# Optimization experiments

Hardware: AMD Instinct MI355X
Metric: run time of the kernel (lower is better)

Reference implementation:

```python
import jax, jax.numpy as jnp
import numpy as np

NUM_HEADS = 12
LEVEL = 16
SOFTMAX_STEP = 6.0  # spiking_softmax.step

def _if_init(shape):
    # torch lazily inits q = zeros + 0.5, acc_q = zeros
    return (jnp.full(shape, 0.5, jnp.float32), jnp.zeros(shape, jnp.float32))

def _if_step(state, x, pos_max, neg_min):
    # IFNeuron with q_threshold = 1.0, borrow = 0.0 (all t-branches collapse to q += x.detach())
    q, acc = state
    q = q + jax.lax.stop_gradient(x)
    acc = jnp.round(acc)
    pos = (q - 1.0 >= 0.0) & (acc < pos_max)
    neg = (q < 0.0) & (acc > neg_min)
    out = jnp.where(pos, 1.0, jnp.where(neg, -1.0, 0.0)).astype(jnp.float32)
    return (q - out, acc + out), out

def _forward(x, w_qkv, w_proj):
    T, B, N, C = x.shape
    H = NUM_HEADS
    D = C // H
    scale = D ** -0.5
    pos_s, neg_s = LEVEL // 2 - 1, -(LEVEL // 2)  # sym=True IF neurons
    pos_u, neg_u = LEVEL // 2 - 1, 0              # sym=False (attn_softmax_IF)

    carry = (
        _if_init((B, H, N, D)), _if_init((B, H, N, D)), _if_init((B, H, N, D)),  # q/k/v IF
        _if_init((B, H, N, N)), _if_init((B, H, N, N)),                           # attn IF, softmax IF
        _if_init((B, H, N, D)), _if_init((B, N, C)),                              # after-attn IF, proj IF
        jnp.zeros((B, H, N, N), jnp.float32), jnp.zeros((B, H, N, N), jnp.float32),  # Ssoftmax X, Y_pre
    )

    def step(carry, xs):
        xt, t = xs
        qif, kif, vif, aif, sif, oif, pif, sm_X, sm_Y = carry
        qkv = (xt @ w_qkv.T).reshape(B, N, 3, H, D).transpose(2, 0, 3, 1, 4)  # [3,B,H,N,D]
        qif, q = _if_step(qif, qkv[0], pos_s, neg_s)
        kif, k = _if_step(kif, qkv[1], pos_s, neg_s)
        vif, v = _if_step(vif, qkv[2], pos_s, neg_s)
        q_s = q * scale
        q_acc = qif[1] * scale  # acc_q * scale * q_threshold (thr=1)
        k_acc = kif[1]
        # AttentionMulti incremental-sum QK^T: q_sum@k^T + q@k_sum^T - q@k^T
        attn = (jnp.einsum('bhnd,bhmd->bhnm', q_acc, k)
                + jnp.einsum('bhnd,bhmd->bhnm', q_s, k_acc)
                - jnp.einsum('bhnd,bhmd->bhnm', q_s, k))
        aif, attn = _if_step(aif, attn, pos_s, neg_s)
        # spiking_softmax: delta of (scaled) softmax over accumulated logits
        sm_X = sm_X + attn
        Y = jax.nn.softmax(sm_X, axis=-1) * jnp.minimum(t / SOFTMAX_STEP, 1.0)
        attn = Y - sm_Y
        sm_Y = Y
        sif, attn = _if_step(sif, attn, pos_u, neg_u)
        # AttentionMulti1 incremental-sum attn@V: a_sum@v + a@v_sum - a@v
        out = (jnp.einsum('bhnm,bhmd->bhnd', sif[1], v)
               + jnp.einsum('bhnm,bhmd->bhnd', attn, vif[1])
               - jnp.einsum('bhnm,bhmd->bhnd', attn, v))
        oif, out = _if_step(oif, out, pos_s, neg_s)
        out = out.transpose(0, 2, 1, 3).reshape(B, N, C) @ w_proj.T
        pif, out = _if_step(pif, out, pos_s, neg_s)
        return (qif, kif, vif, aif, sif, oif, pif, sm_X, sm_Y), out

    ts = jnp.arange(1, T + 1, dtype=jnp.float32)
    _, ys = jax.lax.scan(step, carry, (x, ts))
    return ys  # [T, B, N, C] spike outputs per timestep

def setup_inputs():
    key = jax.random.key(0)
    k1, k2, k3 = jax.random.split(key, 3)
    T, B, N, C = 8, 8, 512, 768
    x = jax.random.normal(k1, (T, B, N, C), jnp.float32)
    w_qkv = jax.random.normal(k2, (3 * C, C), jnp.float32) / np.sqrt(C)
    w_proj = jax.random.normal(k3, (C, C), jnp.float32) / np.sqrt(C)
    return {"x": x, "w_qkv": w_qkv, "w_proj": w_proj}

def reference(x, w_qkv, w_proj):
    return _forward(x, w_qkv, w_proj)
```

## Files before the change

### kernel.cpp

```cpp
#include <hip/hip_runtime.h>
#include <stdint.h>

typedef __attribute__((ext_vector_type(4))) float f32x4;
typedef __attribute__((ext_vector_type(8))) short s16x8;
typedef __attribute__((ext_vector_type(8))) char  s8x8;
typedef __attribute__((ext_vector_type(16))) char s8x16;
typedef unsigned short u16;

constexpr int    Tn  = 8;
constexpr int    Nn  = 512;
constexpr int    Cn  = 768;
constexpr int    Dn  = 64;
constexpr int    BHn = 96;
constexpr int    BNn = 4096;
constexpr int    C3n = 2304;
constexpr size_t BHND = 3145728;
constexpr size_t BHNN = 25165824;
constexpr size_t BNC  = 3145728;

__device__ int8_t g_A1[(size_t)Tn * BHND * 2];
__device__ int8_t g_B1[(size_t)Tn * BHND * 2];
__device__ short  g_S16[(size_t)Tn * BHNN];
__device__ int8_t g_v8 [(size_t)Tn * BHND];
__device__ int8_t g_vd8[(size_t)Tn * BHND];
__device__ int8_t g_vT[(size_t)Tn * BHn * Dn * 1024];
__device__ int8_t g_sifa8[(size_t)Tn * BHNN];
__device__ int8_t g_spk8[(size_t)Tn * BHNN];
__device__ short  g_pv16[(size_t)Tn * BHND];
__device__ int8_t g_osp8i[(size_t)BNn * Tn * Cn];

static __device__ __forceinline__ u16 f2bf(float f) {
    union { float f; unsigned int u; } v; v.f = f;
    return (u16)(v.u >> 16);
}

static __device__ __forceinline__ s16x8 cvt_i8_bf16x8(const int8_t* p) {
    s8x8 v = *(const s8x8*)p;
    s16x8 r;
#pragma unroll
    for (int j = 0; j < 8; ++j) r[j] = (short)f2bf((float)v[j]);
    return r;
}

static __device__ __forceinline__ void st2i8(int8_t* p, int v0, int v1) {
    *(short*)p = (short)((v0 & 0xff) | (v1 << 8));
}

static __device__ __forceinline__ float if_sym(float x, float& q, int& a) {
    float q2 = q + x;
    bool pos = ((q2 - 1.0f) >= 0.0f) && (a < 7);
    bool neg = (q2 < 0.0f) && (a > -8);
    float out = pos ? 1.0f : (neg ? -1.0f : 0.0f);
    q = q2 - out;
    a += (int)out;
    return out;
}

__global__ __launch_bounds__(256) void gemm_qkv_fused(
    const float* __restrict__ X, const float* __restrict__ B)
{
    __shared__ __align__(16) float As[16][132];
    __shared__ __align__(16) float Bs[16][100];
    const int tid = threadIdx.x;
    const int m0 = blockIdx.y * 128;
    const int j0 = blockIdx.x * 96;
    const int ty = tid >> 4, tx = tid & 15;

    float acc[8][6];
#pragma unroll
    for (int i = 0; i < 8; ++i)
#pragma unroll
        for (int j = 0; j < 6; ++j) acc[i][j] = 0.0f;

    for (int k0 = 0; k0 < Cn; k0 += 16) {
#pragma unroll
        for (int u = 0; u < 2; ++u) {
            int f = tid + u * 256;
            int row = f >> 2;
            int c4 = (f & 3) * 4;
            int m = m0 + row;
            int t = m & 7, bn = m >> 3;
            int b = bn >> 9, n = bn & 511;
            const float* xr = X + ((size_t)((t * 8 + b) * Nn + n)) * Cn;
            float4 av = *(const float4*)(xr + k0 + c4);
            As[c4 + 0][row] = av.x; As[c4 + 1][row] = av.y;
            As[c4 + 2][row] = av.z; As[c4 + 3][row] = av.w;
        }
#pragma unroll
        for (int u = 0; u < 3; ++u) {
            int f = tid + u * 256;
            int row = f >> 3;
            int c2 = (f & 7) * 2;
            float2 bv = *(const float2*)(B + (size_t)(j0 + row) * Cn + k0 + c2);
            Bs[c2][row] = bv.x; Bs[c2 + 1][row] = bv.y;
        }
        __syncthreads();
#pragma unroll
        for (int k = 0; k < 16; ++k) {
            alignas(16) float a[8];
            alignas(8)  float b[6];
            *(float4*)(a)     = *(const float4*)&As[k][ty * 8];
            *(float4*)(a + 4) = *(const float4*)&As[k][ty * 8 + 4];
#pragma unroll
            for (int u = 0; u < 3; ++u) {
                float2 t = *(const float2*)&Bs[k][tx * 2 + 32 * u];
                b[2 * u] = t.x; b[2 * u + 1] = t.y;
            }
#pragma unroll
            for (int i = 0; i < 8; ++i)
#pragma unroll
                for (int j = 0; j < 6; ++j)
                    acc[i][j] = fmaf(a[i], b[j], acc[i][j]);
        }
        __syncthreads();
    }

    const int type = (j0 >= 1536) ? 2 : ((j0 >= 768) ? 1 : 0);
    const int bn = (m0 + ty * 8) >> 3;
    const int b = bn >> 9, n = bn & 511;
#pragma unroll
    for (int u = 0; u < 3; ++u) {
        int c  = j0 + 32 * u + tx * 2;
        int cl = c - type * 768;
        int h = cl >> 6, d = cl & 63;
        int bh = b * 12 + h;
        float q0 = 0.5f, q1 = 0.5f;
        int   a0 = 0,    a1 = 0;
#pragma unroll
        for (int t = 0; t < Tn; ++t) {
            float o0 = if_sym(acc[t][2 * u],     q0, a0);
            float o1 = if_sym(acc[t][2 * u + 1], q1, a1);
            if (type == 0) {
                size_t p = (((size_t)t * BHn + bh) * Nn + n) * 128 + d;
                st2i8(&g_A1[p],      a0,      a1);
                st2i8(&g_A1[p + 64], (int)o0, (int)o1);
            } else if (type == 1) {
                size_t p = (((size_t)t * BHn + bh) * Nn + n) * 128 + d;
                st2i8(&g_B1[p],      (int)o0,        (int)o1);
                st2i8(&g_B1[p + 64], a0 - (int)o0,   a1 - (int)o1);
            } else {
                size_t p = (size_t)t * BHND + ((size_t)bh * Nn + n) * 64 + d;
                st2i8(&g_v8[p],  (int)o0,      (int)o1);
                st2i8(&g_vd8[p], a0 - (int)o0, a1 - (int)o1);
            }
        }
    }
}

__global__ __launch_bounds__(256) void vT_build() {
    int bh = blockIdx.x % BHn;
    int t  = blockIdx.x / BHn;
    const int8_t* src0 = g_v8  + (size_t)t * BHND + (size_t)bh * Nn * Dn;
    const int8_t* src1 = g_vd8 + (size_t)t * BHND + (size_t)bh * Nn * Dn;
    int8_t* dst = g_vT + ((size_t)t * BHn + bh) * Dn * 1024;
    __shared__ __align__(16) int8_t tile[64][80];
    int tid = threadIdx.x;

    for (int s = 0; s < 2; ++s) {
        const int8_t* src = s ? src1 : src0;
        int koff = s * 512;
        for (int nb = 0; nb < Nn; nb += 64) {
            {
                int n  = tid >> 2;
                int d0 = (tid & 3) * 16;
                s8x16 v = *(const s8x16*)(src + (size_t)(nb + n) * Dn + d0);
                *(s8x16*)&tile[n][d0] = v;
            }
            __syncthreads();
            {
                int d  = tid >> 2;
                int n0 = (tid & 3) * 16;
                s8x16 o;
#pragma unroll
                for (int j = 0; j < 16; ++j) o[j] = tile[n0 + j][d];
                *(s8x16*)(dst + (size_t)d * 1024 + koff + nb + n0) = o;
            }
            __syncthreads();
        }
    }
}

__global__ __launch_bounds__(256) void gemm_attn_all() {
    int t = blockIdx.z;
    int bh = blockIdx.y;
    int tm = blockIdx.x >> 3, tn = blockIdx.x & 7;
    int wave = threadIdx.x >> 6, lane = threadIdx.x & 63;
    int wr = wave >> 1, wc = wave & 1;
    int row0 = tm * 64 + wr * 32, col0 = tn * 64 + wc * 32;
    const int8_t* Ab = g_A1 + ((size_t)t * BHn + bh) * Nn * 128;
    const int8_t* Bb = g_B1 + ((size_t)t * BHn + bh) * Nn * 128;
    int lr = lane & 15, kg = (lane >> 4) * 8;
    f32x4 acc[2][2] = {};
#pragma unroll
    for (int kk = 0; kk < 128; kk += 32) {
        s16x8 a0 = cvt_i8_bf16x8(Ab + (size_t)(row0 + lr) * 128 + kk + kg);
        s16x8 a1 = cvt_i8_bf16x8(Ab + (size_t)(row0 + 16 + lr) * 128 + kk + kg);
        s16x8 b0 = cvt_i8_bf16x8(Bb + (size_t)(col0 + lr) * 128 + kk + kg);
        s16x8 b1 = cvt_i8_bf16x8(Bb + (size_t)(col0 + 16 + lr) * 128 + kk + kg);
        acc[0][0] = __builtin_amdgcn_mfma_f32_16x16x32_bf16(a0, b0, acc[0][0], 0, 0, 0);
        acc[0][1] = __builtin_amdgcn_mfma_f32_16x16x32_bf16(a0, b1, acc[0][1], 0, 0, 0);
        acc[1][0] = __builtin_amdgcn_mfma_f32_16x16x32_bf16(a1, b0, acc[1][0], 0, 0, 0);
        acc[1][1] = __builtin_amdgcn_mfma_f32_16x16x32_bf16(a1, b1, acc[1][1], 0, 0, 0);
    }
    short* Sb = g_S16 + (size_t)t * BHNN + (size_t)bh * Nn * Nn;
#pragma unroll
    for (int i = 0; i < 2; ++i)
#pragma unroll
        for (int j = 0; j < 2; ++j)
#pragma unroll
            for (int q = 0; q < 4; ++q) {
                int row = row0 + i * 16 + (lane >> 4) * 4 + q;
                int col = col0 + j * 16 + lr;
                Sb[row * Nn + col] = (short)(int)acc[i][j][q];
            }
}

__global__ __launch_bounds__(256) void attn_pipeline_all() {
    int rowid = blockIdx.x;
    size_t base = (size_t)rowid * Nn;
    int tid = threadIdx.x;
    __shared__ int   redI[4];
    __shared__ float redF[4];

    int   aq8[2]  = {4, 4};
    int   aac[2]  = {0, 0};
    float sq[2]   = {0.5f, 0.5f};
    int   sa[2]   = {0, 0};
    float yold[2] = {0.0f, 0.0f};

    for (int t = 0; t < Tn; ++t) {
        float st = (t + 1) < 6 ? (float)(t + 1) / 6.0f : 1.0f;
        const short* S = g_S16 + (size_t)t * BHNN;

        int X[2];
        int myMax = -128;
#pragma unroll
        for (int u = 0; u < 2; ++u) {
            int c = tid + u * 256;
            int s  = S[base + c];
            int q8 = aq8[u] + s;
            int a  = aac[u];
            bool pos = (q8 >= 8) && (a < 7);
            bool neg = (q8 < 0) && (a > -8);
            int o = pos ? 1 : (neg ? -1 : 0);
            aq8[u] = q8 - (o << 3);
            a += o;
            aac[u] = a;
            X[u] = a;
            myMax = max(myMax, a);
        }
        for (int off = 32; off; off >>= 1) myMax = max(myMax, __shfl_xor(myMax, off));
        if ((tid & 63) == 0) redI[tid >> 6] = myMax;
        __syncthreads();
        int M = max(max(redI[0], redI[1]), max(redI[2], redI[3]));

        float e[2];
        float mySum = 0.0f;
#pragma unroll
        for (int u = 0; u < 2; ++u) { e[u] = expf((float)(X[u] - M)); mySum += e[u]; }
        for (int off = 32; off; off >>= 1) mySum += __shfl_xor(mySum, off);
        if ((tid & 63) == 0) redF[tid >> 6] = mySum;
        __syncthreads();
        float Ssum = (redF[0] + redF[1]) + (redF[2] + redF[3]);

#pragma unroll
        for (int u = 0; u < 2; ++u) {
            int c = tid + u * 256;
            float y = (e[u] / Ssum) * st;
            float dlt = y - yold[u];
            yold[u] = y;
            float q = sq[u] + dlt;
            int a = sa[u];
            bool pos = ((q - 1.0f) >= 0.0f) && (a < 7);
            bool neg = (q < 0.0f) && (a > 0);
            float o = pos ? 1.0f : (neg ? -1.0f : 0.0f);
            sq[u] = q - o;
            a += (int)o;
            sa[u] = a;
            g_sifa8[(size_t)t * BHNN + base + c] = (int8_t)a;
            g_spk8[(size_t)t * BHNN + base + c]  = (int8_t)o;
        }
    }
}

__global__ __launch_bounds__(256) void gemm_pv_all() {
    int t = blockIdx.z;
    int bh = blockIdx.y;
    int tm = blockIdx.x;
    int wave = threadIdx.x >> 6, lane = threadIdx.x & 63;
    int wr = wave >> 1, wc = wave & 1;
    int row0 = tm * 64 + wr * 32, col0 = wc * 32;
    const int8_t* Aa  = g_sifa8 + (size_t)t * BHNN + (size_t)bh * Nn * Nn;
    const int8_t* Asp = g_spk8  + (size_t)t * BHNN + (size_t)bh * Nn * Nn;
    const int8_t* Bb  = g_vT + ((size_t)t * BHn + bh) * Dn * 1024;
    int lr = lane & 15, kg = (lane >> 4) * 8;
    f32x4 acc[2][2] = {};
    for (int kk = 0; kk < 512; kk += 32) {
        s16x8 a0 = cvt_i8_bf16x8(Aa + (size_t)(row0 + lr) * 512 + kk + kg);
        s16x8 a1 = cvt_i8_bf16x8(Aa + (size_t)(row0 + 16 + lr) * 512 + kk + kg);
        s16x8 b0 = cvt_i8_bf16x8(Bb + (size_t)(col0 + lr) * 1024 + kk + kg);
        s16x8 b1 = cvt_i8_bf16x8(Bb + (size_t)(col0 + 16 + lr) * 1024 + kk + kg);
        acc[0][0] = __builtin_amdgcn_mfma_f32_16x16x32_bf16(a0, b0, acc[0][0], 0, 0, 0);
        acc[0][1] = __builtin_amdgcn_mfma_f32_16x16x32_bf16(a0, b1, acc[0][1], 0, 0, 0);
        acc[1][0] = __builtin_amdgcn_mfma_f32_16x16x32_bf16(a1, b0, acc[1][0], 0, 0, 0);
        acc[1][1] = __builtin_amdgcn_mfma_f32_16x16x32_bf16(a1, b1, acc[1][1], 0, 0, 0);
    }
    for (int kk = 0; kk < 512; kk += 32) {
        s16x8 a0 = cvt_i8_bf16x8(Asp + (size_t)(row0 + lr) * 512 + kk + kg);
        s16x8 a1 = cvt_i8_bf16x8(Asp + (size_t)(row0 + 16 + lr) * 512 + kk + kg);
        s16x8 b0 = cvt_i8_bf16x8(Bb + (size_t)(col0 + lr) * 1024 + 512 + kk + kg);
        s16x8 b1 = cvt_i8_bf16x8(Bb + (size_t)(col0 + 16 + lr) * 1024 + 512 + kk + kg);
        acc[0][0] = __builtin_amdgcn_mfma_f32_16x16x32_bf16(a0, b0, acc[0][0], 0, 0, 0);
        acc[0][1] = __builtin_amdgcn_mfma_f32_16x16x32_bf16(a0, b1, acc[0][1], 0, 0, 0);
        acc[1][0] = __builtin_amdgcn_mfma_f32_16x16x32_bf16(a1, b0, acc[1][0], 0, 0, 0);
        acc[1][1] = __builtin_amdgcn_mfma_f32_16x16x32_bf16(a1, b1, acc[1][1], 0, 0, 0);
    }
    short* Pb = g_pv16 + (size_t)t * BHND + (size_t)bh * Nn * Dn;
#pragma unroll
    for (int i = 0; i < 2; ++i)
#pragma unroll
        for (int j = 0; j < 2; ++j)
#pragma unroll
            for (int q = 0; q < 4; ++q) {
                int row = row0 + i * 16 + (lane >> 4) * 4 + q;
                int col = col0 + j * 16 + lr;
                Pb[row * Dn + col] = (short)(int)acc[i][j][q];
            }
}

__global__ __launch_bounds__(256) void oif_all() {
    int idx = blockIdx.x * 256 + threadIdx.x;
    int d = idx & 63;
    int n = (idx >> 6) & 511;
    int bh = idx >> 15;
    int b = bh / 12, h = bh - b * 12;
    size_t bn = (size_t)(b * Nn + n);
    int c = h * 64 + d;

    float q = 0.5f; int a = 0;
    for (int t = 0; t < Tn; ++t) {
        float x = (float)g_pv16[(size_t)t * BHND + idx];
        float o = if_sym(x, q, a);
        g_osp8i[(bn * 8 + t) * Cn + c] = (int8_t)o;
    }
}

__global__ __launch_bounds__(256) void gemm_proj_pif_all(
    const float* __restrict__ B, float* __restrict__ outp)
{
    __shared__ __align__(16) float As[16][132];
    __shared__ __align__(16) float Bs[16][100];
    const int tid = threadIdx.x;
    const int m0 = blockIdx.y * 128;
    const int j0 = blockIdx.x * 96;
    const int ty = tid >> 4, tx = tid & 15;

    float acc[8][6];
#pragma unroll
    for (int i = 0; i < 8; ++i)
#pragma unroll
        for (int j = 0; j < 6; ++j) acc[i][j] = 0.0f;

    for (int k0 = 0; k0 < Cn; k0 += 16) {
        {
            int row = tid >> 1;
            int c8 = (tid & 1) * 8;
            s8x8 v = *(const s8x8*)(g_osp8i + (size_t)(m0 + row) * Cn + k0 + c8);
#pragma unroll
            for (int j = 0; j < 8; ++j) As[c8 + j][row] = (float)v[j];
        }
#pragma unroll
        for (int u = 0; u < 3; ++u) {
            int f = tid + u * 256;
            int r2 = f >> 3;
            int c2 = (f & 7) * 2;
            float2 bv = *(const float2*)(B + (size_t)(j0 + r2) * Cn + k0 + c2);
            Bs[c2][r2] = bv.x; Bs[c2 + 1][r2] = bv.y;
        }
        __syncthreads();
#pragma unroll
        for (int k = 0; k < 16; ++k) {
            alignas(16) float a[8];
            alignas(8)  float b[6];
            *(float4*)(a)     = *(const float4*)&As[k][ty * 8];
            *(float4*)(a + 4) = *(const float4*)&As[k][ty * 8 + 4];
#pragma unroll
            for (int u = 0; u < 3; ++u) {
                float2 t = *(const float2*)&Bs[k][tx * 2 + 32 * u];
                b[2 * u] = t.x; b[2 * u + 1] = t.y;
            }
#pragma unroll
            for (int i = 0; i < 8; ++i)
#pragma unroll
                for (int j = 0; j < 6; ++j)
                    acc[i][j] = fmaf(a[i], b[j], acc[i][j]);
        }
        __syncthreads();
    }

    const size_t bn = (size_t)((m0 + ty * 8) >> 3);
#pragma unroll
    for (int u = 0; u < 3; ++u) {
        size_t cbase = bn * Cn + j0 + 32 * u + tx * 2;
        float q0 = 0.5f, q1 = 0.5f;
        int   a0 = 0,    a1 = 0;
#pragma unroll
        for (int t = 0; t < Tn; ++t) {
            float o0 = if_sym(acc[t][2 * u],     q0, a0);
            float o1 = if_sym(acc[t][2 * u + 1], q1, a1);
            float2 st; st.x = o0; st.y = o1;
            *(float2*)(outp + (size_t)t * BNC + cbase) = st;
        }
    }
}

extern "C" void kernel_launch(void* const* d_in, const int* in_sizes, int n_in,
                              void* d_out, int out_size, void* d_ws, size_t ws_size,
                              hipStream_t stream) {
    (void)in_sizes; (void)n_in; (void)out_size; (void)d_ws; (void)ws_size;
    const float* x      = (const float*)d_in[0];
    const float* w_qkv  = (const float*)d_in[1];
    const float* w_proj = (const float*)d_in[2];
    float* outp = (float*)d_out;

    gemm_qkv_fused<<<dim3(C3n / 96, (Tn * BNn) / 128), 256, 0, stream>>>(x, w_qkv);
    vT_build<<<Tn * BHn, 256, 0, stream>>>();
    gemm_attn_all<<<dim3(64, BHn, Tn), 256, 0, stream>>>();
    attn_pipeline_all<<<BHn * Nn, 256, 0, stream>>>();
    gemm_pv_all<<<dim3(8, BHn, Tn), 256, 0, stream>>>();
    oif_all<<<(int)(BHND / 256), 256, 0, stream>>>();
    gemm_proj_pif_all<<<dim3(Cn / 96, (Tn * BNn) / 128), 256, 0, stream>>>(w_proj, outp);
}
```

Before: 2.994 ms.

## Use int8 MFMA for attention GEMMs and fuse PV with output IF neuron

Both the QK^T and attn@V GEMMs now feed int8 operands directly to the 16x16x64 i8 MFMA with int32 accumulation, removing the per-element int8-to-bf16 conversion and halving the MFMA count per K. The PV GEMM is also fused with the after-attention IF neuron: each block loops over all timesteps, keeps the neuron state in registers, and writes spikes straight to the projection input. This removes the g_pv16 intermediate and one launch. The cost is that the fused grid shrinks to 768 blocks with a serial time loop, which lowers parallelism for that stage.

New measurement: 2.689 ms (median of 2 runs). 10.2% less time.

```diff
diff --git a/kernel.cpp b/kernel.cpp
--- a/kernel.cpp
+++ b/kernel.cpp
@@ -2,7 +2,7 @@
 #include <stdint.h>
 
 typedef __attribute__((ext_vector_type(4))) float f32x4;
-typedef __attribute__((ext_vector_type(8))) short s16x8;
+typedef __attribute__((ext_vector_type(4))) int   i32x4;
 typedef __attribute__((ext_vector_type(8))) char  s8x8;
 typedef __attribute__((ext_vector_type(16))) char s8x16;
 typedef unsigned short u16;
@@ -18,29 +18,15 @@
 constexpr size_t BHNN = 25165824;
 constexpr size_t BNC  = 3145728;
 
-__device__ int8_t g_A1[(size_t)Tn * BHND * 2];
-__device__ int8_t g_B1[(size_t)Tn * BHND * 2];
-__device__ short  g_S16[(size_t)Tn * BHNN];
-__device__ int8_t g_v8 [(size_t)Tn * BHND];
-__device__ int8_t g_vd8[(size_t)Tn * BHND];
-__device__ int8_t g_vT[(size_t)Tn * BHn * Dn * 1024];
-__device__ int8_t g_sifa8[(size_t)Tn * BHNN];
-__device__ int8_t g_spk8[(size_t)Tn * BHNN];
-__device__ short  g_pv16[(size_t)Tn * BHND];
-__device__ int8_t g_osp8i[(size_t)BNn * Tn * Cn];
-
-static __device__ __forceinline__ u16 f2bf(float f) {
-    union { float f; unsigned int u; } v; v.f = f;
-    return (u16)(v.u >> 16);
-}
-
-static __device__ __forceinline__ s16x8 cvt_i8_bf16x8(const int8_t* p) {
-    s8x8 v = *(const s8x8*)p;
-    s16x8 r;
-#pragma unroll
-    for (int j = 0; j < 8; ++j) r[j] = (short)f2bf((float)v[j]);
-    return r;
-}
+__device__ __attribute__((aligned(16))) int8_t g_A1[(size_t)Tn * BHND * 2];
+__device__ __attribute__((aligned(16))) int8_t g_B1[(size_t)Tn * BHND * 2];
+__device__ __attribute__((aligned(16))) short  g_S16[(size_t)Tn * BHNN];
+__device__ __attribute__((aligned(16))) int8_t g_v8 [(size_t)Tn * BHND];
+__device__ __attribute__((aligned(16))) int8_t g_vd8[(size_t)Tn * BHND];
+__device__ __attribute__((aligned(16))) int8_t g_vT[(size_t)Tn * BHn * Dn * 1024];
+__device__ __attribute__((aligned(16))) int8_t g_sifa8[(size_t)Tn * BHNN];
+__device__ __attribute__((aligned(16))) int8_t g_spk8[(size_t)Tn * BHNN];
+__device__ __attribute__((aligned(16))) int8_t g_osp8i[(size_t)BNn * Tn * Cn];
 
 static __device__ __forceinline__ void st2i8(int8_t* p, int v0, int v1) {
     *(short*)p = (short)((v0 & 0xff) | (v1 << 8));
@@ -136,8 +122,8 @@
                 st2i8(&g_A1[p + 64], (int)o0, (int)o1);
             } else if (type == 1) {
                 size_t p = (((size_t)t * BHn + bh) * Nn + n) * 128 + d;
-                st2i8(&g_B1[p],      (int)o0,        (int)o1);
-                st2i8(&g_B1[p + 64], a0 - (int)o0,   a1 - (int)o1);
+                st2i8(&g_B1[p],      (int)o0,      (int)o1);
+                st2i8(&g_B1[p + 64], a0 - (int)o0, a1 - (int)o1);
             } else {
                 size_t p = (size_t)t * BHND + ((size_t)bh * Nn + n) * 64 + d;
                 st2i8(&g_v8[p],  (int)o0,      (int)o1);
@@ -189,18 +175,18 @@
     int row0 = tm * 64 + wr * 32, col0 = tn * 64 + wc * 32;
     const int8_t* Ab = g_A1 + ((size_t)t * BHn + bh) * Nn * 128;
     const int8_t* Bb = g_B1 + ((size_t)t * BHn + bh) * Nn * 128;
-    int lr = lane & 15, kg = (lane >> 4) * 8;
-    f32x4 acc[2][2] = {};
-#pragma unroll
-    for (int kk = 0; kk < 128; kk += 32) {
-        s16x8 a0 = cvt_i8_bf16x8(Ab + (size_t)(row0 + lr) * 128 + kk + kg);
-        s16x8 a1 = cvt_i8_bf16x8(Ab + (size_t)(row0 + 16 + lr) * 128 + kk + kg);
-        s16x8 b0 = cvt_i8_bf16x8(Bb + (size_t)(col0 + lr) * 128 + kk + kg);
-        s16x8 b1 = cvt_i8_bf16x8(Bb + (size_t)(col0 + 16 + lr) * 128 + kk + kg);
-        acc[0][0] = __builtin_amdgcn_mfma_f32_16x16x32_bf16(a0, b0, acc[0][0], 0, 0, 0);
-        acc[0][1] = __builtin_amdgcn_mfma_f32_16x16x32_bf16(a0, b1, acc[0][1], 0, 0, 0);
-        acc[1][0] = __builtin_amdgcn_mfma_f32_16x16x32_bf16(a1, b0, acc[1][0], 0, 0, 0);
-        acc[1][1] = __builtin_amdgcn_mfma_f32_16x16x32_bf16(a1, b1, acc[1][1], 0, 0, 0);
+    int lr = lane & 15, kg = (lane >> 4) * 16;
+    i32x4 acc[2][2] = {};
+#pragma unroll
+    for (int kk = 0; kk < 128; kk += 64) {
+        i32x4 a0 = *(const i32x4*)(Ab + (size_t)(row0 + lr) * 128 + kk + kg);
+        i32x4 a1 = *(const i32x4*)(Ab + (size_t)(row0 + 16 + lr) * 128 + kk + kg);
+        i32x4 b0 = *(const i32x4*)(Bb + (size_t)(col0 + lr) * 128 + kk + kg);
+        i32x4 b1 = *(const i32x4*)(Bb + (size_t)(col0 + 16 + lr) * 128 + kk + kg);
+        acc[0][0] = __builtin_amdgcn_mfma_i32_16x16x64_i8(a0, b0, acc[0][0], 0, 0, 0);
+        acc[0][1] = __builtin_amdgcn_mfma_i32_16x16x64_i8(a0, b1, acc[0][1], 0, 0, 0);
+        acc[1][0] = __builtin_amdgcn_mfma_i32_16x16x64_i8(a1, b0, acc[1][0], 0, 0, 0);
+        acc[1][1] = __builtin_amdgcn_mfma_i32_16x16x64_i8(a1, b1, acc[1][1], 0, 0, 0);
     }
     short* Sb = g_S16 + (size_t)t * BHNN + (size_t)bh * Nn * Nn;
 #pragma unroll
@@ -211,7 +197,7 @@
             for (int q = 0; q < 4; ++q) {
                 int row = row0 + i * 16 + (lane >> 4) * 4 + q;
                 int col = col0 + j * 16 + lr;
-                Sb[row * Nn + col] = (short)(int)acc[i][j][q];
+                Sb[row * Nn + col] = (short)acc[i][j][q];
             }
 }
 
@@ -283,65 +269,62 @@
     }
 }
 
-__global__ __launch_bounds__(256) void gemm_pv_all() {
-    int t = blockIdx.z;
+__global__ __launch_bounds__(256) void gemm_pv_oif_all() {
     int bh = blockIdx.y;
     int tm = blockIdx.x;
     int wave = threadIdx.x >> 6, lane = threadIdx.x & 63;
     int wr = wave >> 1, wc = wave & 1;
     int row0 = tm * 64 + wr * 32, col0 = wc * 32;
-    const int8_t* Aa  = g_sifa8 + (size_t)t * BHNN + (size_t)bh * Nn * Nn;
-    const int8_t* Asp = g_spk8  + (size_t)t * BHNN + (size_t)bh * Nn * Nn;
-    const int8_t* Bb  = g_vT + ((size_t)t * BHn + bh) * Dn * 1024;
-    int lr = lane & 15, kg = (lane >> 4) * 8;
-    f32x4 acc[2][2] = {};
-    for (int kk = 0; kk < 512; kk += 32) {
-        s16x8 a0 = cvt_i8_bf16x8(Aa + (size_t)(row0 + lr) * 512 + kk + kg);
-        s16x8 a1 = cvt_i8_bf16x8(Aa + (size_t)(row0 + 16 + lr) * 512 + kk + kg);
-        s16x8 b0 = cvt_i8_bf16x8(Bb + (size_t)(col0 + lr) * 1024 + kk + kg);
-        s16x8 b1 = cvt_i8_bf16x8(Bb + (size_t)(col0 + 16 + lr) * 1024 + kk + kg);
-        acc[0][0] = __builtin_amdgcn_mfma_f32_16x16x32_bf16(a0, b0, acc[0][0], 0, 0, 0);
-        acc[0][1] = __builtin_amdgcn_mfma_f32_16x16x32_bf16(a0, b1, acc[0][1], 0, 0, 0);
-        acc[1][0] = __builtin_amdgcn_mfma_f32_16x16x32_bf16(a1, b0, acc[1][0], 0, 0, 0);
-        acc[1][1] = __builtin_amdgcn_mfma_f32_16x16x32_bf16(a1, b1, acc[1][1], 0, 0, 0);
-    }
-    for (int kk = 0; kk < 512; kk += 32) {
-        s16x8 a0 = cvt_i8_bf16x8(Asp + (size_t)(row0 + lr) * 512 + kk + kg);
-        s16x8 a1 = cvt_i8_bf16x8(Asp + (size_t)(row0 + 16 + lr) * 512 + kk + kg);
-        s16x8 b0 = cvt_i8_bf16x8(Bb + (size_t)(col0 + lr) * 1024 + 512 + kk + kg);
-        s16x8 b1 = cvt_i8_bf16x8(Bb + (size_t)(col0 + 16 + lr) * 1024 + 512 + kk + kg);
-        acc[0][0] = __builtin_amdgcn_mfma_f32_16x16x32_bf16(a0, b0, acc[0][0], 0, 0, 0);
-        acc[0][1] = __builtin_amdgcn_mfma_f32_16x16x32_bf16(a0, b1, acc[0][1], 0, 0, 0);
-        acc[1][0] = __builtin_amdgcn_mfma_f32_16x16x32_bf16(a1, b0, acc[1][0], 0, 0, 0);
-        acc[1][1] = __builtin_amdgcn_mfma_f32_16x16x32_bf16(a1, b1, acc[1][1], 0, 0, 0);
-    }
-    short* Pb = g_pv16 + (size_t)t * BHND + (size_t)bh * Nn * Dn;
+    int lr = lane & 15, kg = (lane >> 4) * 16;
+    int b = bh / 12, h = bh - b * 12;
+
+    float oq[2][2][4];
+    int   oa[2][2][4];
 #pragma unroll
     for (int i = 0; i < 2; ++i)
 #pragma unroll
         for (int j = 0; j < 2; ++j)
 #pragma unroll
-            for (int q = 0; q < 4; ++q) {
-                int row = row0 + i * 16 + (lane >> 4) * 4 + q;
-                int col = col0 + j * 16 + lr;
-                Pb[row * Dn + col] = (short)(int)acc[i][j][q];
-            }
-}
-
-__global__ __launch_bounds__(256) void oif_all() {
-    int idx = blockIdx.x * 256 + threadIdx.x;
-    int d = idx & 63;
-    int n = (idx >> 6) & 511;
-    int bh = idx >> 15;
-    int b = bh / 12, h = bh - b * 12;
-    size_t bn = (size_t)(b * Nn + n);
-    int c = h * 64 + d;
-
-    float q = 0.5f; int a = 0;
+            for (int q = 0; q < 4; ++q) { oq[i][j][q] = 0.5f; oa[i][j][q] = 0; }
+
     for (int t = 0; t < Tn; ++t) {
-        float x = (float)g_pv16[(size_t)t * BHND + idx];
-        float o = if_sym(x, q, a);
-        g_osp8i[(bn * 8 + t) * Cn + c] = (int8_t)o;
+        const int8_t* Aa  = g_sifa8 + (size_t)t * BHNN + (size_t)bh * Nn * Nn;
+        const int8_t* Asp = g_spk8  + (size_t)t * BHNN + (size_t)bh * Nn * Nn;
+        const int8_t* Bb  = g_vT + ((size_t)t * BHn + bh) * Dn * 1024;
+        i32x4 acc[2][2] = {};
+        for (int kk = 0; kk < 512; kk += 64) {
+            i32x4 a0 = *(const i32x4*)(Aa + (size_t)(row0 + lr) * 512 + kk + kg);
+            i32x4 a1 = *(const i32x4*)(Aa + (size_t)(row0 + 16 + lr) * 512 + kk + kg);
+            i32x4 b0 = *(const i32x4*)(Bb + (size_t)(col0 + lr) * 1024 + kk + kg);
+            i32x4 b1 = *(const i32x4*)(Bb + (size_t)(col0 + 16 + lr) * 1024 + kk + kg);
+            acc[0][0] = __builtin_amdgcn_mfma_i32_16x16x64_i8(a0, b0, acc[0][0], 0, 0, 0);
+            acc[0][1] = __builtin_amdgcn_mfma_i32_16x16x64_i8(a0, b1, acc[0][1], 0, 0, 0);
+            acc[1][0] = __builtin_amdgcn_mfma_i32_16x16x64_i8(a1, b0, acc[1][0], 0, 0, 0);
+            acc[1][1] = __builtin_amdgcn_mfma_i32_16x16x64_i8(a1, b1, acc[1][1], 0, 0, 0);
+        }
+        for (int kk = 0; kk < 512; kk += 64) {
+            i32x4 a0 = *(const i32x4*)(Asp + (size_t)(row0 + lr) * 512 + kk + kg);
+            i32x4 a1 = *(const i32x4*)(Asp + (size_t)(row0 + 16 + lr) * 512 + kk + kg);
+            i32x4 b0 = *(const i32x4*)(Bb + (size_t)(col0 + lr) * 1024 + 512 + kk + kg);
+            i32x4 b1 = *(const i32x4*)(Bb + (size_t)(col0 + 16 + lr) * 1024 + 512 + kk + kg);
+            acc[0][0] = __builtin_amdgcn_mfma_i32_16x16x64_i8(a0, b0, acc[0][0], 0, 0, 0);
+            acc[0][1] = __builtin_amdgcn_mfma_i32_16x16x64_i8(a0, b1, acc[0][1], 0, 0, 0);
+            acc[1][0] = __builtin_amdgcn_mfma_i32_16x16x64_i8(a1, b0, acc[1][0], 0, 0, 0);
+            acc[1][1] = __builtin_amdgcn_mfma_i32_16x16x64_i8(a1, b1, acc[1][1], 0, 0, 0);
+        }
+#pragma unroll
+        for (int i = 0; i < 2; ++i)
+#pragma unroll
+            for (int j = 0; j < 2; ++j)
+#pragma unroll
+                for (int q = 0; q < 4; ++q) {
+                    int row = row0 + i * 16 + (lane >> 4) * 4 + q;
+                    int col = col0 + j * 16 + lr;
+                    float x = (float)acc[i][j][q];
+                    float o = if_sym(x, oq[i][j][q], oa[i][j][q]);
+                    size_t bn = (size_t)(b * Nn + row);
+                    g_osp8i[(bn * 8 + t) * Cn + h * 64 + col] = (int8_t)o;
+                }
     }
 }
 
@@ -427,7 +410,6 @@
     vT_build<<<Tn * BHn, 256, 0, stream>>>();
     gemm_attn_all<<<dim3(64, BHn, Tn), 256, 0, stream>>>();
     attn_pipeline_all<<<BHn * Nn, 256, 0, stream>>>();
-    gemm_pv_all<<<dim3(8, BHn, Tn), 256, 0, stream>>>();
-    oif_all<<<(int)(BHND / 256), 256, 0, stream>>>();
+    gemm_pv_oif_all<<<dim3(8, BHn), 256, 0, stream>>>();
     gemm_proj_pif_all<<<dim3(Cn / 96, (Tn * BNn) / 128), 256, 0, stream>>>(w_proj, outp);
 }
```
